# Performance work log

Hardware: AMD Instinct MI355X
Metric: run time of the kernel (lower is better)

## Reference

```python
import jax, jax.numpy as jnp
import numpy as np

N = 50000
E = 400000
IN_DIM = 16
EMB = 32
HID = 128
HEADS = 4
LAYERS = 3
EPS_BN = 1e-5
NEG_SLOPE = 0.2


def setup_inputs() -> dict:
    key = jax.random.key(0)
    ks = jax.random.split(key, 16)
    s = 0.1
    C = HID  # per-head out channels (concat=False)
    inp = {
        "x": jax.random.normal(ks[0], (N, IN_DIM), jnp.float32),
        "edge_index": jax.random.randint(ks[1], (2, E), 0, N, jnp.int64),
        "emb": s * jax.random.normal(ks[2], (N, EMB), jnp.float32),
        "Wf": s * jax.random.normal(ks[3], (EMB, IN_DIM), jnp.float32),
        "bf": jnp.zeros((EMB,), jnp.float32),
        "Wc": s * jax.random.normal(ks[4], (HID, 2 * EMB), jnp.float32),
        "bc": jnp.zeros((HID,), jnp.float32),
        "Wl": s * jax.random.normal(ks[5], (LAYERS, HEADS * C, HID), jnp.float32),
        "a_src": s * jax.random.normal(ks[6], (LAYERS, HEADS, C), jnp.float32),
        "a_dst": s * jax.random.normal(ks[7], (LAYERS, HEADS, C), jnp.float32),
        "bl": jnp.zeros((LAYERS, C), jnp.float32),
        "gamma": jnp.ones((LAYERS, C), jnp.float32),
        "beta": jnp.zeros((LAYERS, C), jnp.float32),
        "Wout": s * jax.random.normal(ks[8], (1, HID), jnp.float32),
        "bout": jnp.zeros((1,), jnp.float32),
    }
    return inp


def _gat_layer(h, src, dst, W, a_s, a_d, b):
    n = h.shape[0]
    C = W.shape[0] // HEADS
    hp = (h @ W.T).reshape(n, HEADS, C)                # (N,H,C)
    al_s = jnp.sum(hp * a_s, axis=-1)                  # (N,H)
    al_d = jnp.sum(hp * a_d, axis=-1)                  # (N,H)
    e = jax.nn.leaky_relu(al_s[src] + al_d[dst], NEG_SLOPE)  # (E,H)
    m = jax.ops.segment_max(e, dst, num_segments=n)    # per-target max
    ex = jnp.exp(e - m[dst])
    denom = jax.ops.segment_sum(ex, dst, num_segments=n) + 1e-16
    alpha = ex / denom[dst]                            # (E,H)
    msg = hp[src] * alpha[..., None]                   # (E,H,C)
    out = jax.ops.segment_sum(msg, dst, num_segments=n)
    return jnp.mean(out, axis=1) + b                   # concat=False: head mean


def _bn(x, g, b):
    mu = jnp.mean(x, axis=0)
    var = jnp.var(x, axis=0)  # biased, as torch BN uses for normalization
    return (x - mu) * jax.lax.rsqrt(var + EPS_BN) * g + b


def reference(x, edge_index, emb, Wf, bf, Wc, bc, Wl, a_src, a_dst, bl, gamma, beta, Wout, bout):
    n = x.shape[0]
    loop = jnp.arange(n, dtype=edge_index.dtype)
    src = jnp.concatenate([edge_index[0], loop])       # add self loops
    dst = jnp.concatenate([edge_index[1], loop])
    feat = x @ Wf.T + bf
    h = jax.nn.relu(jnp.concatenate([emb, feat], axis=1) @ Wc.T + bc)
    prev_h = h
    for i in range(LAYERS):
        h = _gat_layer(h, src, dst, Wl[i], a_src[i], a_dst[i], bl[i])
        h = jax.nn.relu(_bn(h, gamma[i], beta[i]))
        if prev_h.shape == h.shape:
            h = h + prev_h
        prev_h = h
    out = h @ Wout.T + bout
    return jnp.clip(out, -10.0, 10.0)
```

## Files before the change

kernel.cpp:

```cpp
#include <hip/hip_runtime.h>
#include <hip/hip_bf16.h>
#include <math.h>

#define INDIM 16
#define EMBD 32
#define UDIM 64
#define HIDD 128
#define HEADS 4
#define LAYERS 3
#define MPAD 50048

typedef short v8s __attribute__((ext_vector_type(8)));
typedef float v4f __attribute__((ext_vector_type(4)));

__device__ __forceinline__ float lrelu(float x) { return x > 0.f ? x : 0.2f * x; }
__device__ __forceinline__ float bf2f(unsigned int bits16) {
    unsigned int u = bits16 << 16;
    return __builtin_bit_cast(float, u);
}
__device__ __forceinline__ unsigned short f2bf(float f) {
    unsigned int u = __builtin_bit_cast(unsigned int, f);
    unsigned int lsb = (u >> 16) & 1;
    u += 0x7fff + lsb;
    return (unsigned short)(u >> 16);
}

__global__ __launch_bounds__(256) void k_enc(const float* __restrict__ x,
                                             const float* __restrict__ emb,
                                             const float* __restrict__ Wf,
                                             const float* __restrict__ bf,
                                             unsigned short* __restrict__ u, int n) {
    int i = blockIdx.x * 256 + threadIdx.x;
    if (i >= n * EMBD) return;
    int node = i >> 5, j = i & 31;
    const float* xr = x + (size_t)node * INDIM;
    const float* wr = Wf + (size_t)j * INDIM;
    float s = bf[j];
#pragma unroll
    for (int k = 0; k < INDIM; k++) s += xr[k] * wr[k];
    u[(size_t)node * UDIM + EMBD + j] = f2bf(s);
    u[(size_t)node * UDIM + j] = f2bf(emb[(size_t)node * EMBD + j]);
}

__global__ __launch_bounds__(256) void k_prep_v(const float* __restrict__ Wl,
                                                unsigned short* __restrict__ Vb) {
    int i = blockIdx.x * 256 + threadIdx.x;
    if (i >= LAYERS * HIDD * 512) return;
    int l = i >> 16;
    int rem = i & 65535;
    int c = rem >> 9;
    int f = rem & 511;
    int h = f >> 7, k = f & 127;
    Vb[i] = f2bf(Wl[(size_t)l * 512 * HIDD + (size_t)(h * HIDD + c) * HIDD + k]);
}

__global__ __launch_bounds__(256) void k_prep_a(const float* __restrict__ Wl,
                                                const float* __restrict__ a_s,
                                                const float* __restrict__ a_d,
                                                float* __restrict__ ws, float* __restrict__ wd) {
    int i = blockIdx.x * 256 + threadIdx.x;
    if (i >= LAYERS * HEADS * HIDD) return;
    int l = i >> 9, h = (i >> 7) & 3, k = i & 127;
    const float* W = Wl + (size_t)l * 512 * HIDD;
    const float* as = a_s + l * 512 + h * HIDD;
    const float* ad = a_d + l * 512 + h * HIDD;
    float ss = 0.f, sd = 0.f;
    for (int c = 0; c < HIDD; c++) {
        float w = W[(size_t)(h * HIDD + c) * HIDD + k];
        ss += as[c] * w;
        sd += ad[c] * w;
    }
    ws[i] = ss;
    wd[i] = sd;
}

__global__ __launch_bounds__(256) void k_prep_wc(const float* __restrict__ Wc,
                                                 unsigned short* __restrict__ Wcb) {
    int i = blockIdx.x * 256 + threadIdx.x;
    if (i < HIDD * UDIM) Wcb[i] = f2bf(Wc[i]);
}

template <int K, int EPI>
__global__ __launch_bounds__(256) void k_gemm(const unsigned short* __restrict__ A,
                                              const unsigned short* __restrict__ B,
                                              const float* __restrict__ bias,
                                              float* __restrict__ O,
                                              unsigned short* __restrict__ Ob,
                                              float* __restrict__ bns, int M) {
    int tid = threadIdx.x;
    int lane = tid & 63, wid = tid >> 6;
    int wm = wid >> 1, wn = wid & 1;
    int bm = blockIdx.x * 128;
    int lr = lane & 15, lk = lane >> 4;
    __shared__ float s1[128], s2[128];
    if (EPI == 1) {
        if (tid < 128) { s1[tid] = 0.f; s2[tid] = 0.f; }
        __syncthreads();
    }
    v4f acc[4][4] = {};
    const unsigned short* Abase = A + (size_t)(bm + wm * 64 + lr) * K + lk * 8;
    const unsigned short* Bbase = B + (size_t)(wn * 64 + lr) * K + lk * 8;
#pragma unroll
    for (int kk = 0; kk < K / 32; kk++) {
        v8s a[4], b[4];
#pragma unroll
        for (int f = 0; f < 4; f++) {
            a[f] = *(const v8s*)(Abase + (size_t)(f * 16) * K + kk * 32);
            b[f] = *(const v8s*)(Bbase + (size_t)(f * 16) * K + kk * 32);
        }
#pragma unroll
        for (int i = 0; i < 4; i++)
#pragma unroll
            for (int j = 0; j < 4; j++)
                acc[i][j] = __builtin_amdgcn_mfma_f32_16x16x32_bf16(a[i], b[j], acc[i][j], 0, 0, 0);
    }
#pragma unroll
    for (int i = 0; i < 4; i++) {
#pragma unroll
        for (int r = 0; r < 4; r++) {
            int row = bm + wm * 64 + i * 16 + lk * 4 + r;
            if (EPI == 0 && row >= M) continue;
#pragma unroll
            for (int j = 0; j < 4; j++) {
                int col = wn * 64 + j * 16 + lr;
                float v = acc[i][j][r];
                if (EPI == 0) {
                    v = fmaxf(v + bias[col], 0.f);
                    O[(size_t)row * HIDD + col] = v;
                    Ob[(size_t)row * HIDD + col] = f2bf(v);
                } else {
                    O[(size_t)row * HIDD + col] = v;
                }
            }
        }
    }
    if (EPI == 1) {
#pragma unroll
        for (int j = 0; j < 4; j++) {
            int col = wn * 64 + j * 16 + lr;
            float ls = 0.f, lq = 0.f;
#pragma unroll
            for (int i = 0; i < 4; i++)
#pragma unroll
                for (int r = 0; r < 4; r++) {
                    float v = acc[i][j][r];
                    ls += v;
                    lq += v * v;
                }
            atomicAdd(&s1[col], ls);
            atomicAdd(&s2[col], lq);
        }
        __syncthreads();
        if (tid < 128) {
            atomicAdd(&bns[tid], s1[tid]);
            atomicAdd(&bns[128 + tid], s2[tid]);
        }
    }
}

__global__ __launch_bounds__(256) void k_deg(const int* __restrict__ ei, int* __restrict__ deg,
                                             int E, int tot) {
    int e = blockIdx.x * 256 + threadIdx.x;
    if (e >= tot) return;
    int dst = (e < E) ? ei[E + e] : (e - E);
    atomicAdd(&deg[dst], 1);
}

__global__ __launch_bounds__(256) void k_scan1(const int* __restrict__ deg,
                                               int* __restrict__ rowptr,
                                               int* __restrict__ partials, int n) {
    int tid = threadIdx.x;
    int i = blockIdx.x * 256 + tid;
    int v = (i < n) ? deg[i] : 0;
    __shared__ int sm[256];
    sm[tid] = v;
    __syncthreads();
    for (int off = 1; off < 256; off <<= 1) {
        int t = (tid >= off) ? sm[tid - off] : 0;
        __syncthreads();
        sm[tid] += t;
        __syncthreads();
    }
    if (i < n) rowptr[i] = sm[tid] - v;
    if (tid == 255) partials[blockIdx.x] = sm[255];
}

__global__ __launch_bounds__(256) void k_scan2(int* __restrict__ partials, int nb) {
    int tid = threadIdx.x;
    int v = (tid < nb) ? partials[tid] : 0;
    __shared__ int sm[256];
    sm[tid] = v;
    __syncthreads();
    for (int off = 1; off < 256; off <<= 1) {
        int t = (tid >= off) ? sm[tid - off] : 0;
        __syncthreads();
        sm[tid] += t;
        __syncthreads();
    }
    if (tid < nb) partials[tid] = sm[tid] - v;
}

__global__ __launch_bounds__(256) void k_scan3(const int* __restrict__ deg,
                                               const int* __restrict__ partials,
                                               int* __restrict__ rowptr,
                                               int* __restrict__ cursor, int n) {
    int i = blockIdx.x * 256 + threadIdx.x;
    if (i >= n) return;
    int r = rowptr[i] + partials[blockIdx.x];
    rowptr[i] = r;
    cursor[i] = r;
    if (i == n - 1) rowptr[n] = r + deg[i];
}

__global__ __launch_bounds__(256) void k_scatter(const int* __restrict__ ei, int* __restrict__ cursor,
                                                 int* __restrict__ csr_src, int E, int tot) {
    int e = blockIdx.x * 256 + threadIdx.x;
    if (e >= tot) return;
    int src = (e < E) ? ei[e] : (e - E);
    int dst = (e < E) ? ei[E + e] : (e - E);
    int pos = atomicAdd(&cursor[dst], 1);
    csr_src[pos] = src;
}

__global__ __launch_bounds__(256) void k_al0(const float* __restrict__ h,
                                             const float* __restrict__ ws,
                                             const float* __restrict__ wd,
                                             float* __restrict__ al_s, float* __restrict__ al_d,
                                             int n) {
    int wid = threadIdx.x >> 6, lane = threadIdx.x & 63;
    int node = blockIdx.x * 4 + wid;
    if (node >= n) return;
    float2 v = *(const float2*)(h + (size_t)node * HIDD + 2 * lane);
    float s[8];
#pragma unroll
    for (int hh = 0; hh < 4; hh++) {
        float2 w1 = *(const float2*)(ws + hh * HIDD + 2 * lane);
        float2 w2 = *(const float2*)(wd + hh * HIDD + 2 * lane);
        s[hh] = v.x * w1.x + v.y * w1.y;
        s[4 + hh] = v.x * w2.x + v.y * w2.y;
    }
#pragma unroll
    for (int o = 32; o; o >>= 1)
#pragma unroll
        for (int q = 0; q < 8; q++) s[q] += __shfl_xor(s[q], o);
    if (lane == 0) {
        *(float4*)(al_s + (size_t)node * 4) = make_float4(s[0], s[1], s[2], s[3]);
        *(float4*)(al_d + (size_t)node * 4) = make_float4(s[4], s[5], s[6], s[7]);
    }
}

__global__ __launch_bounds__(256) void k_attngat(const int* __restrict__ rowptr,
                                                 const int* __restrict__ csr_src,
                                                 const float* __restrict__ al_s,
                                                 const float* __restrict__ al_d,
                                                 const unsigned short* __restrict__ hb,
                                                 unsigned short* __restrict__ g, int n) {
    int wid = threadIdx.x >> 6, lane = threadIdx.x & 63;
    int node = blockIdx.x * 4 + wid;
    if (node >= n) return;
    int start = rowptr[node], end = rowptr[node + 1];
    int deg = end - start;
    const float4* als4 = (const float4*)al_s;
    float4 ad = ((const float4*)al_d)[node];
    const unsigned int* h2 = (const unsigned int*)hb;
    float acc[4][2] = {};

    if (deg <= 64) {
        bool act = lane < deg;
        int src_l = act ? csr_src[start + lane] : 0;
        float e0 = -3.0e38f, e1 = -3.0e38f, e2 = -3.0e38f, e3 = -3.0e38f;
        if (act) {
            float4 as = als4[src_l];
            e0 = lrelu(as.x + ad.x);
            e1 = lrelu(as.y + ad.y);
            e2 = lrelu(as.z + ad.z);
            e3 = lrelu(as.w + ad.w);
        }
        float m0 = e0, m1 = e1, m2 = e2, m3 = e3;
#pragma unroll
        for (int o = 32; o; o >>= 1) {
            m0 = fmaxf(m0, __shfl_xor(m0, o));
            m1 = fmaxf(m1, __shfl_xor(m1, o));
            m2 = fmaxf(m2, __shfl_xor(m2, o));
            m3 = fmaxf(m3, __shfl_xor(m3, o));
        }
        float p0 = act ? expf(e0 - m0) : 0.f;
        float p1 = act ? expf(e1 - m1) : 0.f;
        float p2 = act ? expf(e2 - m2) : 0.f;
        float p3 = act ? expf(e3 - m3) : 0.f;
        float t0 = p0, t1 = p1, t2 = p2, t3 = p3;
#pragma unroll
        for (int o = 32; o; o >>= 1) {
            t0 += __shfl_xor(t0, o);
            t1 += __shfl_xor(t1, o);
            t2 += __shfl_xor(t2, o);
            t3 += __shfl_xor(t3, o);
        }
        float a0 = p0 / (t0 + 1e-16f), a1 = p1 / (t1 + 1e-16f);
        float a2 = p2 / (t2 + 1e-16f), a3 = p3 / (t3 + 1e-16f);
        for (int jj = 0; jj < deg; jj++) {
            int sj = __shfl(src_l, jj);
            float b0 = __shfl(a0, jj), b1 = __shfl(a1, jj);
            float b2 = __shfl(a2, jj), b3 = __shfl(a3, jj);
            unsigned int uu = h2[(size_t)sj * 64 + lane];
            float x0 = bf2f(uu & 0xffff), x1 = bf2f(uu >> 16);
            acc[0][0] += b0 * x0; acc[0][1] += b0 * x1;
            acc[1][0] += b1 * x0; acc[1][1] += b1 * x1;
            acc[2][0] += b2 * x0; acc[2][1] += b2 * x1;
            acc[3][0] += b3 * x0; acc[3][1] += b3 * x1;
        }
    } else {
        float m0 = -3.0e38f, m1 = -3.0e38f, m2 = -3.0e38f, m3 = -3.0e38f;
        for (int j = start + lane; j < end; j += 64) {
            float4 as = als4[csr_src[j]];
            m0 = fmaxf(m0, lrelu(as.x + ad.x));
            m1 = fmaxf(m1, lrelu(as.y + ad.y));
            m2 = fmaxf(m2, lrelu(as.z + ad.z));
            m3 = fmaxf(m3, lrelu(as.w + ad.w));
        }
#pragma unroll
        for (int o = 32; o; o >>= 1) {
            m0 = fmaxf(m0, __shfl_xor(m0, o));
            m1 = fmaxf(m1, __shfl_xor(m1, o));
            m2 = fmaxf(m2, __shfl_xor(m2, o));
            m3 = fmaxf(m3, __shfl_xor(m3, o));
        }
        float t0 = 0.f, t1 = 0.f, t2 = 0.f, t3 = 0.f;
        for (int j = start + lane; j < end; j += 64) {
            float4 as = als4[csr_src[j]];
            t0 += expf(lrelu(as.x + ad.x) - m0);
            t1 += expf(lrelu(as.y + ad.y) - m1);
            t2 += expf(lrelu(as.z + ad.z) - m2);
            t3 += expf(lrelu(as.w + ad.w) - m3);
        }
#pragma unroll
        for (int o = 32; o; o >>= 1) {
            t0 += __shfl_xor(t0, o);
            t1 += __shfl_xor(t1, o);
            t2 += __shfl_xor(t2, o);
            t3 += __shfl_xor(t3, o);
        }
        float i0 = 1.f / (t0 + 1e-16f), i1 = 1.f / (t1 + 1e-16f);
        float i2 = 1.f / (t2 + 1e-16f), i3 = 1.f / (t3 + 1e-16f);
        for (int base = start; base < end; base += 64) {
            int cnt = min(64, end - base);
            bool act = lane < cnt;
            int src_l = act ? csr_src[base + lane] : 0;
            float a0 = 0.f, a1 = 0.f, a2 = 0.f, a3 = 0.f;
            if (act) {
                float4 as = als4[src_l];
                a0 = expf(lrelu(as.x + ad.x) - m0) * i0;
                a1 = expf(lrelu(as.y + ad.y) - m1) * i1;
                a2 = expf(lrelu(as.z + ad.z) - m2) * i2;
                a3 = expf(lrelu(as.w + ad.w) - m3) * i3;
            }
            for (int jj = 0; jj < cnt; jj++) {
                int sj = __shfl(src_l, jj);
                float b0 = __shfl(a0, jj), b1 = __shfl(a1, jj);
                float b2 = __shfl(a2, jj), b3 = __shfl(a3, jj);
                unsigned int uu = h2[(size_t)sj * 64 + lane];
                float x0 = bf2f(uu & 0xffff), x1 = bf2f(uu >> 16);
                acc[0][0] += b0 * x0; acc[0][1] += b0 * x1;
                acc[1][0] += b1 * x0; acc[1][1] += b1 * x1;
                acc[2][0] += b2 * x0; acc[2][1] += b2 * x1;
                acc[3][0] += b3 * x0; acc[3][1] += b3 * x1;
            }
        }
    }
    unsigned int* g2 = (unsigned int*)g;
#pragma unroll
    for (int hh = 0; hh < 4; hh++) {
        unsigned int p = (unsigned int)f2bf(acc[hh][0]) | ((unsigned int)f2bf(acc[hh][1]) << 16);
        g2[(size_t)node * 256 + hh * 64 + lane] = p;
    }
}

template <int MODE>
__global__ __launch_bounds__(256) void k_apply(const float* __restrict__ agg,
                                               const float* __restrict__ bns,
                                               const float* __restrict__ gamma,
                                               const float* __restrict__ beta,
                                               float* __restrict__ h,
                                               unsigned short* __restrict__ hb,
                                               const float* __restrict__ ws,
                                               const float* __restrict__ wd,
                                               float* __restrict__ al_s,
                                               float* __restrict__ al_d,
                                               const float* __restrict__ Wout,
                                               const float* __restrict__ bout,
                                               float* __restrict__ out,
                                               float invn, int n) {
    int wid = threadIdx.x >> 6, lane = threadIdx.x & 63;
    int node = blockIdx.x * 4 + wid;
    if (node >= n) return;
    int c0 = 2 * lane, c1 = 2 * lane + 1;
    float2 ag = *(const float2*)(agg + (size_t)node * HIDD + c0);
    float2 ho = *(const float2*)(h + (size_t)node * HIDD + c0);
    float mu0 = bns[c0] * invn, mu1 = bns[c1] * invn;
    float va0 = bns[128 + c0] * invn - mu0 * mu0;
    float va1 = bns[128 + c1] * invn - mu1 * mu1;
    float sc0 = gamma[c0] * rsqrtf(0.0625f * va0 + 1e-5f);
    float sc1 = gamma[c1] * rsqrtf(0.0625f * va1 + 1e-5f);
    float v0 = fmaxf((ag.x - mu0) * 0.25f * sc0 + beta[c0], 0.f) + ho.x;
    float v1 = fmaxf((ag.y - mu1) * 0.25f * sc1 + beta[c1], 0.f) + ho.y;
    if (MODE == 0) {
        *(float2*)(h + (size_t)node * HIDD + c0) = make_float2(v0, v1);
        ((unsigned int*)hb)[(size_t)node * 64 + lane] =
            (unsigned int)f2bf(v0) | ((unsigned int)f2bf(v1) << 16);
        float s[8];
#pragma unroll
        for (int hh = 0; hh < 4; hh++) {
            float2 w1 = *(const float2*)(ws + hh * HIDD + c0);
            float2 w2 = *(const float2*)(wd + hh * HIDD + c0);
            s[hh] = v0 * w1.x + v1 * w1.y;
            s[4 + hh] = v0 * w2.x + v1 * w2.y;
        }
#pragma unroll
        for (int o = 32; o; o >>= 1)
#pragma unroll
            for (int q = 0; q < 8; q++) s[q] += __shfl_xor(s[q], o);
        if (lane == 0) {
            *(float4*)(al_s + (size_t)node * 4) = make_float4(s[0], s[1], s[2], s[3]);
            *(float4*)(al_d + (size_t)node * 4) = make_float4(s[4], s[5], s[6], s[7]);
        }
    } else {
        float2 w = *(const float2*)(Wout + c0);
        float p = v0 * w.x + v1 * w.y;
#pragma unroll
        for (int o = 32; o; o >>= 1) p += __shfl_xor(p, o);
        if (lane == 0) {
            float v = p + bout[0];
            out[node] = fminf(fmaxf(v, -10.f), 10.f);
        }
    }
}

extern "C" void kernel_launch(void* const* d_in, const int* in_sizes, int n_in,
                              void* d_out, int out_size, void* d_ws, size_t ws_size,
                              hipStream_t stream) {
    const float* x = (const float*)d_in[0];
    const int* ei = (const int*)d_in[1];
    const float* emb = (const float*)d_in[2];
    const float* Wf = (const float*)d_in[3];
    const float* bf = (const float*)d_in[4];
    const float* Wc = (const float*)d_in[5];
    const float* bc = (const float*)d_in[6];
    const float* Wl = (const float*)d_in[7];
    const float* a_src = (const float*)d_in[8];
    const float* a_dst = (const float*)d_in[9];
    const float* gamma = (const float*)d_in[11];
    const float* beta = (const float*)d_in[12];
    const float* Wout = (const float*)d_in[13];
    const float* bout = (const float*)d_in[14];
    float* out = (float*)d_out;

    int n = in_sizes[0] / INDIM;
    int E = in_sizes[1] / 2;
    int tot = E + n;
    int NB = (n + 255) / 256;

    size_t off = 0;
    auto alloc = [&](size_t bytes) {
        void* p = (char*)d_ws + off;
        off = (off + bytes + 255) & ~(size_t)255;
        return p;
    };
    unsigned short* u = (unsigned short*)alloc((size_t)MPAD * UDIM * 2);
    float* h = (float*)alloc((size_t)MPAD * HIDD * 4);
    unsigned short* hb = (unsigned short*)alloc((size_t)MPAD * HIDD * 2);
    unsigned short* g = (unsigned short*)alloc((size_t)MPAD * 512 * 2);
    float* agg = (float*)alloc((size_t)MPAD * HIDD * 4);
    float* al_s = (float*)alloc((size_t)n * HEADS * 4);
    float* al_d = (float*)alloc((size_t)n * HEADS * 4);
    int* deg = (int*)alloc((size_t)n * 4);
    int* rowptr = (int*)alloc(((size_t)n + 1) * 4);
    int* cursor = (int*)alloc((size_t)n * 4);
    int* csr_src = (int*)alloc((size_t)tot * 4);
    int* partials = (int*)alloc((size_t)NB * 4);
    unsigned short* Vb = (unsigned short*)alloc((size_t)LAYERS * HIDD * 512 * 2);
    unsigned short* Wcb = (unsigned short*)alloc((size_t)HIDD * UDIM * 2);
    float* ws = (float*)alloc((size_t)LAYERS * HEADS * HIDD * 4);
    float* wd = (float*)alloc((size_t)LAYERS * HEADS * HIDD * 4);
    float* bnsums = (float*)alloc(LAYERS * 256 * 4);
    (void)ws_size;

    hipMemsetAsync(deg, 0, (size_t)n * 4, stream);
    hipMemsetAsync(bnsums, 0, LAYERS * 256 * 4, stream);
    if (n < MPAD) {
        hipMemsetAsync(u + (size_t)n * UDIM, 0, (size_t)(MPAD - n) * UDIM * 2, stream);
        hipMemsetAsync(g + (size_t)n * 512, 0, (size_t)(MPAD - n) * 512 * 2, stream);
    }

    k_prep_v<<<(LAYERS * HIDD * 512 + 255) / 256, 256, 0, stream>>>(Wl, Vb);
    k_prep_a<<<(LAYERS * HEADS * HIDD + 255) / 256, 256, 0, stream>>>(Wl, a_src, a_dst, ws, wd);
    k_prep_wc<<<(HIDD * UDIM + 255) / 256, 256, 0, stream>>>(Wc, Wcb);

    k_deg<<<(tot + 255) / 256, 256, 0, stream>>>(ei, deg, E, tot);
    k_scan1<<<NB, 256, 0, stream>>>(deg, rowptr, partials, n);
    k_scan2<<<1, 256, 0, stream>>>(partials, NB);
    k_scan3<<<NB, 256, 0, stream>>>(deg, partials, rowptr, cursor, n);
    k_scatter<<<(tot + 255) / 256, 256, 0, stream>>>(ei, cursor, csr_src, E, tot);

    k_enc<<<(n * EMBD + 255) / 256, 256, 0, stream>>>(x, emb, Wf, bf, u, n);
    k_gemm<UDIM, 0><<<MPAD / 128, 256, 0, stream>>>(u, Wcb, bc, h, hb, nullptr, n);
    k_al0<<<(n + 3) / 4, 256, 0, stream>>>(h, ws, wd, al_s, al_d, n);

    float invn = 1.0f / (float)n;
    for (int l = 0; l < LAYERS; l++) {
        k_attngat<<<(n + 3) / 4, 256, 0, stream>>>(rowptr, csr_src, al_s, al_d, hb, g, n);
        k_gemm<512, 1><<<MPAD / 128, 256, 0, stream>>>(g, Vb + (size_t)l * HIDD * 512, nullptr,
                                                       agg, nullptr, bnsums + l * 256, MPAD);
        if (l < LAYERS - 1)
            k_apply<0><<<(n + 3) / 4, 256, 0, stream>>>(
                agg, bnsums + l * 256, gamma + l * HIDD, beta + l * HIDD, h, hb,
                ws + (size_t)(l + 1) * 512, wd + (size_t)(l + 1) * 512, al_s, al_d,
                nullptr, nullptr, nullptr, invn, n);
        else
            k_apply<1><<<(n + 3) / 4, 256, 0, stream>>>(
                agg, bnsums + l * 256, gamma + l * HIDD, beta + l * HIDD, h, hb,
                nullptr, nullptr, nullptr, nullptr, Wout, bout, out, invn, n);
    }
}
```

Measured before the change: 486.3 us.

## Fuse GAT attention aggregation with projection GEMM through shared memory

Merges the attention-aggregation kernel and the per-layer 512-wide projection GEMM into a single kernel. Each block aggregates 16 nodes into a bf16 tile in LDS, then multiplies it by the weight matrix with MFMA and accumulates the batch-norm statistics. This removes the round trip of the N×512 bf16 intermediate through global memory and one launch per layer. The neighbor gather loop is also unrolled by two to raise memory-level parallelism. In exchange, the weight matrix is re-read from global/L2 by every 16-row block, the MFMA tile is small, and the per-block BN atomics grow because there are many more blocks.

```diff
diff --git a/kernel.cpp b/kernel.cpp
--- a/kernel.cpp
+++ b/kernel.cpp
@@ -80,23 +80,17 @@
     if (i < HIDD * UDIM) Wcb[i] = f2bf(Wc[i]);
 }
 
-template <int K, int EPI>
-__global__ __launch_bounds__(256) void k_gemm(const unsigned short* __restrict__ A,
-                                              const unsigned short* __restrict__ B,
-                                              const float* __restrict__ bias,
-                                              float* __restrict__ O,
-                                              unsigned short* __restrict__ Ob,
-                                              float* __restrict__ bns, int M) {
+__global__ __launch_bounds__(256) void k_gemm_enc(const unsigned short* __restrict__ A,
+                                                  const unsigned short* __restrict__ B,
+                                                  const float* __restrict__ bias,
+                                                  float* __restrict__ O,
+                                                  unsigned short* __restrict__ Ob, int M) {
+    const int K = UDIM;
     int tid = threadIdx.x;
     int lane = tid & 63, wid = tid >> 6;
     int wm = wid >> 1, wn = wid & 1;
     int bm = blockIdx.x * 128;
     int lr = lane & 15, lk = lane >> 4;
-    __shared__ float s1[128], s2[128];
-    if (EPI == 1) {
-        if (tid < 128) { s1[tid] = 0.f; s2[tid] = 0.f; }
-        __syncthreads();
-    }
     v4f acc[4][4] = {};
     const unsigned short* Abase = A + (size_t)(bm + wm * 64 + lr) * K + lk * 8;
     const unsigned short* Bbase = B + (size_t)(wn * 64 + lr) * K + lk * 8;
@@ -119,41 +113,14 @@
 #pragma unroll
         for (int r = 0; r < 4; r++) {
             int row = bm + wm * 64 + i * 16 + lk * 4 + r;
-            if (EPI == 0 && row >= M) continue;
+            if (row >= M) continue;
 #pragma unroll
             for (int j = 0; j < 4; j++) {
                 int col = wn * 64 + j * 16 + lr;
-                float v = acc[i][j][r];
-                if (EPI == 0) {
-                    v = fmaxf(v + bias[col], 0.f);
-                    O[(size_t)row * HIDD + col] = v;
-                    Ob[(size_t)row * HIDD + col] = f2bf(v);
-                } else {
-                    O[(size_t)row * HIDD + col] = v;
-                }
+                float v = fmaxf(acc[i][j][r] + bias[col], 0.f);
+                O[(size_t)row * HIDD + col] = v;
+                Ob[(size_t)row * HIDD + col] = f2bf(v);
             }
-        }
-    }
-    if (EPI == 1) {
-#pragma unroll
-        for (int j = 0; j < 4; j++) {
-            int col = wn * 64 + j * 16 + lr;
-            float ls = 0.f, lq = 0.f;
-#pragma unroll
-            for (int i = 0; i < 4; i++)
-#pragma unroll
-                for (int r = 0; r < 4; r++) {
-                    float v = acc[i][j][r];
-                    ls += v;
-                    lq += v * v;
-                }
-            atomicAdd(&s1[col], ls);
-            atomicAdd(&s2[col], lq);
-        }
-        __syncthreads();
-        if (tid < 128) {
-            atomicAdd(&bns[tid], s1[tid]);
-            atomicAdd(&bns[128 + tid], s2[tid]);
         }
     }
 }
@@ -249,129 +216,189 @@
     }
 }
 
-__global__ __launch_bounds__(256) void k_attngat(const int* __restrict__ rowptr,
-                                                 const int* __restrict__ csr_src,
-                                                 const float* __restrict__ al_s,
-                                                 const float* __restrict__ al_d,
-                                                 const unsigned short* __restrict__ hb,
-                                                 unsigned short* __restrict__ g, int n) {
-    int wid = threadIdx.x >> 6, lane = threadIdx.x & 63;
-    int node = blockIdx.x * 4 + wid;
-    if (node >= n) return;
-    int start = rowptr[node], end = rowptr[node + 1];
-    int deg = end - start;
+__global__ __launch_bounds__(256) void k_layer(const int* __restrict__ rowptr,
+                                               const int* __restrict__ csr_src,
+                                               const float* __restrict__ al_s,
+                                               const float* __restrict__ al_d,
+                                               const unsigned short* __restrict__ hb,
+                                               const unsigned short* __restrict__ Vb,
+                                               float* __restrict__ agg,
+                                               float* __restrict__ bns, int n) {
+    __shared__ unsigned short G[16][520];
+    __shared__ float s1[128], s2[128];
+    int tid = threadIdx.x, lane = tid & 63, wid = tid >> 6;
+    if (tid < 128) { s1[tid] = 0.f; s2[tid] = 0.f; }
+    int node0 = blockIdx.x * 16;
     const float4* als4 = (const float4*)al_s;
-    float4 ad = ((const float4*)al_d)[node];
     const unsigned int* h2 = (const unsigned int*)hb;
-    float acc[4][2] = {};
-
-    if (deg <= 64) {
-        bool act = lane < deg;
-        int src_l = act ? csr_src[start + lane] : 0;
-        float e0 = -3.0e38f, e1 = -3.0e38f, e2 = -3.0e38f, e3 = -3.0e38f;
-        if (act) {
-            float4 as = als4[src_l];
-            e0 = lrelu(as.x + ad.x);
-            e1 = lrelu(as.y + ad.y);
-            e2 = lrelu(as.z + ad.z);
-            e3 = lrelu(as.w + ad.w);
-        }
-        float m0 = e0, m1 = e1, m2 = e2, m3 = e3;
-#pragma unroll
-        for (int o = 32; o; o >>= 1) {
-            m0 = fmaxf(m0, __shfl_xor(m0, o));
-            m1 = fmaxf(m1, __shfl_xor(m1, o));
-            m2 = fmaxf(m2, __shfl_xor(m2, o));
-            m3 = fmaxf(m3, __shfl_xor(m3, o));
-        }
-        float p0 = act ? expf(e0 - m0) : 0.f;
-        float p1 = act ? expf(e1 - m1) : 0.f;
-        float p2 = act ? expf(e2 - m2) : 0.f;
-        float p3 = act ? expf(e3 - m3) : 0.f;
-        float t0 = p0, t1 = p1, t2 = p2, t3 = p3;
-#pragma unroll
-        for (int o = 32; o; o >>= 1) {
-            t0 += __shfl_xor(t0, o);
-            t1 += __shfl_xor(t1, o);
-            t2 += __shfl_xor(t2, o);
-            t3 += __shfl_xor(t3, o);
-        }
-        float a0 = p0 / (t0 + 1e-16f), a1 = p1 / (t1 + 1e-16f);
-        float a2 = p2 / (t2 + 1e-16f), a3 = p3 / (t3 + 1e-16f);
-        for (int jj = 0; jj < deg; jj++) {
-            int sj = __shfl(src_l, jj);
-            float b0 = __shfl(a0, jj), b1 = __shfl(a1, jj);
-            float b2 = __shfl(a2, jj), b3 = __shfl(a3, jj);
-            unsigned int uu = h2[(size_t)sj * 64 + lane];
-            float x0 = bf2f(uu & 0xffff), x1 = bf2f(uu >> 16);
-            acc[0][0] += b0 * x0; acc[0][1] += b0 * x1;
-            acc[1][0] += b1 * x0; acc[1][1] += b1 * x1;
-            acc[2][0] += b2 * x0; acc[2][1] += b2 * x1;
-            acc[3][0] += b3 * x0; acc[3][1] += b3 * x1;
-        }
-    } else {
-        float m0 = -3.0e38f, m1 = -3.0e38f, m2 = -3.0e38f, m3 = -3.0e38f;
-        for (int j = start + lane; j < end; j += 64) {
-            float4 as = als4[csr_src[j]];
-            m0 = fmaxf(m0, lrelu(as.x + ad.x));
-            m1 = fmaxf(m1, lrelu(as.y + ad.y));
-            m2 = fmaxf(m2, lrelu(as.z + ad.z));
-            m3 = fmaxf(m3, lrelu(as.w + ad.w));
-        }
-#pragma unroll
-        for (int o = 32; o; o >>= 1) {
-            m0 = fmaxf(m0, __shfl_xor(m0, o));
-            m1 = fmaxf(m1, __shfl_xor(m1, o));
-            m2 = fmaxf(m2, __shfl_xor(m2, o));
-            m3 = fmaxf(m3, __shfl_xor(m3, o));
-        }
-        float t0 = 0.f, t1 = 0.f, t2 = 0.f, t3 = 0.f;
-        for (int j = start + lane; j < end; j += 64) {
-            float4 as = als4[csr_src[j]];
-            t0 += expf(lrelu(as.x + ad.x) - m0);
-            t1 += expf(lrelu(as.y + ad.y) - m1);
-            t2 += expf(lrelu(as.z + ad.z) - m2);
-            t3 += expf(lrelu(as.w + ad.w) - m3);
-        }
-#pragma unroll
-        for (int o = 32; o; o >>= 1) {
-            t0 += __shfl_xor(t0, o);
-            t1 += __shfl_xor(t1, o);
-            t2 += __shfl_xor(t2, o);
-            t3 += __shfl_xor(t3, o);
-        }
-        float i0 = 1.f / (t0 + 1e-16f), i1 = 1.f / (t1 + 1e-16f);
-        float i2 = 1.f / (t2 + 1e-16f), i3 = 1.f / (t3 + 1e-16f);
-        for (int base = start; base < end; base += 64) {
-            int cnt = min(64, end - base);
-            bool act = lane < cnt;
-            int src_l = act ? csr_src[base + lane] : 0;
-            float a0 = 0.f, a1 = 0.f, a2 = 0.f, a3 = 0.f;
-            if (act) {
-                float4 as = als4[src_l];
-                a0 = expf(lrelu(as.x + ad.x) - m0) * i0;
-                a1 = expf(lrelu(as.y + ad.y) - m1) * i1;
-                a2 = expf(lrelu(as.z + ad.z) - m2) * i2;
-                a3 = expf(lrelu(as.w + ad.w) - m3) * i3;
+    unsigned int* Gw = (unsigned int*)G;
+
+    for (int i = 0; i < 4; i++) {
+        int lrow = wid * 4 + i;
+        int node = node0 + lrow;
+        float acc[4][2] = {};
+        if (node < n) {
+            int start = rowptr[node], end = rowptr[node + 1];
+            int deg = end - start;
+            float4 ad = ((const float4*)al_d)[node];
+            if (deg <= 64) {
+                bool act = lane < deg;
+                int src_l = act ? csr_src[start + lane] : 0;
+                float e0 = -3.0e38f, e1 = -3.0e38f, e2 = -3.0e38f, e3 = -3.0e38f;
+                if (act) {
+                    float4 as = als4[src_l];
+                    e0 = lrelu(as.x + ad.x);
+                    e1 = lrelu(as.y + ad.y);
+                    e2 = lrelu(as.z + ad.z);
+                    e3 = lrelu(as.w + ad.w);
+                }
+                float m0 = e0, m1 = e1, m2 = e2, m3 = e3;
+#pragma unroll
+                for (int o = 32; o; o >>= 1) {
+                    m0 = fmaxf(m0, __shfl_xor(m0, o));
+                    m1 = fmaxf(m1, __shfl_xor(m1, o));
+                    m2 = fmaxf(m2, __shfl_xor(m2, o));
+                    m3 = fmaxf(m3, __shfl_xor(m3, o));
+                }
+                float p0 = act ? expf(e0 - m0) : 0.f;
+                float p1 = act ? expf(e1 - m1) : 0.f;
+                float p2 = act ? expf(e2 - m2) : 0.f;
+                float p3 = act ? expf(e3 - m3) : 0.f;
+                float t0 = p0, t1 = p1, t2 = p2, t3 = p3;
+#pragma unroll
+                for (int o = 32; o; o >>= 1) {
+                    t0 += __shfl_xor(t0, o);
+                    t1 += __shfl_xor(t1, o);
+                    t2 += __shfl_xor(t2, o);
+                    t3 += __shfl_xor(t3, o);
+                }
+                float a0 = p0 / (t0 + 1e-16f), a1 = p1 / (t1 + 1e-16f);
+                float a2 = p2 / (t2 + 1e-16f), a3 = p3 / (t3 + 1e-16f);
+                int jj = 0;
+                for (; jj + 2 <= deg; jj += 2) {
+                    int sj0 = __shfl(src_l, jj), sj1 = __shfl(src_l, jj + 1);
+                    unsigned int u0 = h2[(size_t)sj0 * 64 + lane];
+                    unsigned int u1 = h2[(size_t)sj1 * 64 + lane];
+                    float b00 = __shfl(a0, jj), b01 = __shfl(a1, jj);
+                    float b02 = __shfl(a2, jj), b03 = __shfl(a3, jj);
+                    float b10 = __shfl(a0, jj + 1), b11 = __shfl(a1, jj + 1);
+                    float b12 = __shfl(a2, jj + 1), b13 = __shfl(a3, jj + 1);
+                    float x00 = bf2f(u0 & 0xffff), x01 = bf2f(u0 >> 16);
+                    float x10 = bf2f(u1 & 0xffff), x11 = bf2f(u1 >> 16);
+                    acc[0][0] += b00 * x00 + b10 * x10; acc[0][1] += b00 * x01 + b10 * x11;
+                    acc[1][0] += b01 * x00 + b11 * x10; acc[1][1] += b01 * x01 + b11 * x11;
+                    acc[2][0] += b02 * x00 + b12 * x10; acc[2][1] += b02 * x01 + b12 * x11;
+                    acc[3][0] += b03 * x00 + b13 * x10; acc[3][1] += b03 * x01 + b13 * x11;
+                }
+                if (jj < deg) {
+                    int sj = __shfl(src_l, jj);
+                    unsigned int uu = h2[(size_t)sj * 64 + lane];
+                    float b0 = __shfl(a0, jj), b1 = __shfl(a1, jj);
+                    float b2 = __shfl(a2, jj), b3 = __shfl(a3, jj);
+                    float x0 = bf2f(uu & 0xffff), x1 = bf2f(uu >> 16);
+                    acc[0][0] += b0 * x0; acc[0][1] += b0 * x1;
+                    acc[1][0] += b1 * x0; acc[1][1] += b1 * x1;
+                    acc[2][0] += b2 * x0; acc[2][1] += b2 * x1;
+                    acc[3][0] += b3 * x0; acc[3][1] += b3 * x1;
+                }
+            } else {
+                float m0 = -3.0e38f, m1 = -3.0e38f, m2 = -3.0e38f, m3 = -3.0e38f;
+                for (int j = start + lane; j < end; j += 64) {
+                    float4 as = als4[csr_src[j]];
+                    m0 = fmaxf(m0, lrelu(as.x + ad.x));
+                    m1 = fmaxf(m1, lrelu(as.y + ad.y));
+                    m2 = fmaxf(m2, lrelu(as.z + ad.z));
+                    m3 = fmaxf(m3, lrelu(as.w + ad.w));
+                }
+#pragma unroll
+                for (int o = 32; o; o >>= 1) {
+                    m0 = fmaxf(m0, __shfl_xor(m0, o));
+                    m1 = fmaxf(m1, __shfl_xor(m1, o));
+                    m2 = fmaxf(m2, __shfl_xor(m2, o));
+                    m3 = fmaxf(m3, __shfl_xor(m3, o));
+                }
+                float t0 = 0.f, t1 = 0.f, t2 = 0.f, t3 = 0.f;
+                for (int j = start + lane; j < end; j += 64) {
+                    float4 as = als4[csr_src[j]];
+                    t0 += expf(lrelu(as.x + ad.x) - m0);
+                    t1 += expf(lrelu(as.y + ad.y) - m1);
+                    t2 += expf(lrelu(as.z + ad.z) - m2);
+                    t3 += expf(lrelu(as.w + ad.w) - m3);
+                }
+#pragma unroll
+                for (int o = 32; o; o >>= 1) {
+                    t0 += __shfl_xor(t0, o);
+                    t1 += __shfl_xor(t1, o);
+                    t2 += __shfl_xor(t2, o);
+                    t3 += __shfl_xor(t3, o);
+                }
+                float i0 = 1.f / (t0 + 1e-16f), i1 = 1.f / (t1 + 1e-16f);
+                float i2 = 1.f / (t2 + 1e-16f), i3 = 1.f / (t3 + 1e-16f);
+                for (int base = start; base < end; base += 64) {
+                    int cnt = min(64, end - base);
+                    bool act = lane < cnt;
+                    int src_l = act ? csr_src[base + lane] : 0;
+                    float a0 = 0.f, a1 = 0.f, a2 = 0.f, a3 = 0.f;
+                    if (act) {
+                        float4 as = als4[src_l];
+                        a0 = expf(lrelu(as.x + ad.x) - m0) * i0;
+                        a1 = expf(lrelu(as.y + ad.y) - m1) * i1;
+                        a2 = expf(lrelu(as.z + ad.z) - m2) * i2;
+                        a3 = expf(lrelu(as.w + ad.w) - m3) * i3;
+                    }
+                    for (int jj = 0; jj < cnt; jj++) {
+                        int sj = __shfl(src_l, jj);
+                        float b0 = __shfl(a0, jj), b1 = __shfl(a1, jj);
+                        float b2 = __shfl(a2, jj), b3 = __shfl(a3, jj);
+                        unsigned int uu = h2[(size_t)sj * 64 + lane];
+                        float x0 = bf2f(uu & 0xffff), x1 = bf2f(uu >> 16);
+                        acc[0][0] += b0 * x0; acc[0][1] += b0 * x1;
+                        acc[1][0] += b1 * x0; acc[1][1] += b1 * x1;
+                        acc[2][0] += b2 * x0; acc[2][1] += b2 * x1;
+                        acc[3][0] += b3 * x0; acc[3][1] += b3 * x1;
+                    }
+                }
             }
-            for (int jj = 0; jj < cnt; jj++) {
-                int sj = __shfl(src_l, jj);
-                float b0 = __shfl(a0, jj), b1 = __shfl(a1, jj);
-                float b2 = __shfl(a2, jj), b3 = __shfl(a3, jj);
-                unsigned int uu = h2[(size_t)sj * 64 + lane];
-                float x0 = bf2f(uu & 0xffff), x1 = bf2f(uu >> 16);
-                acc[0][0] += b0 * x0; acc[0][1] += b0 * x1;
-                acc[1][0] += b1 * x0; acc[1][1] += b1 * x1;
-                acc[2][0] += b2 * x0; acc[2][1] += b2 * x1;
-                acc[3][0] += b3 * x0; acc[3][1] += b3 * x1;
+        }
+#pragma unroll
+        for (int hh = 0; hh < 4; hh++) {
+            unsigned int p = (unsigned int)f2bf(acc[hh][0]) | ((unsigned int)f2bf(acc[hh][1]) << 16);
+            Gw[lrow * 260 + hh * 64 + lane] = p;
+        }
+    }
+    __syncthreads();
+
+    int lr = lane & 15, lk = lane >> 4;
+    v4f acc2[2] = {};
+#pragma unroll
+    for (int kk = 0; kk < 16; kk++) {
+        v8s a = *(const v8s*)((const char*)G + lr * 1040 + kk * 64 + lk * 16);
+        v8s b0 = *(const v8s*)(Vb + (size_t)(wid * 32 + lr) * 512 + kk * 32 + lk * 8);
+        v8s b1 = *(const v8s*)(Vb + (size_t)(wid * 32 + 16 + lr) * 512 + kk * 32 + lk * 8);
+        acc2[0] = __builtin_amdgcn_mfma_f32_16x16x32_bf16(a, b0, acc2[0], 0, 0, 0);
+        acc2[1] = __builtin_amdgcn_mfma_f32_16x16x32_bf16(a, b1, acc2[1], 0, 0, 0);
+    }
+#pragma unroll
+    for (int j = 0; j < 2; j++) {
+        int col = wid * 32 + j * 16 + lr;
+        float ls = 0.f, lq = 0.f;
+#pragma unroll
+        for (int r = 0; r < 4; r++) {
+            int node = node0 + lk * 4 + r;
+            float v = acc2[j][r];
+            if (node < n) {
+                agg[(size_t)node * HIDD + col] = v;
+                ls += v;
+                lq += v * v;
             }
         }
-    }
-    unsigned int* g2 = (unsigned int*)g;
-#pragma unroll
-    for (int hh = 0; hh < 4; hh++) {
-        unsigned int p = (unsigned int)f2bf(acc[hh][0]) | ((unsigned int)f2bf(acc[hh][1]) << 16);
-        g2[(size_t)node * 256 + hh * 64 + lane] = p;
+        atomicAdd(&s1[col], ls);
+        atomicAdd(&s2[col], lq);
+    }
+    __syncthreads();
+    if (tid < 128) {
+        atomicAdd(&bns[tid], s1[tid]);
+        atomicAdd(&bns[128 + tid], s2[tid]);
     }
 }
 
@@ -468,7 +495,6 @@
     unsigned short* u = (unsigned short*)alloc((size_t)MPAD * UDIM * 2);
     float* h = (float*)alloc((size_t)MPAD * HIDD * 4);
     unsigned short* hb = (unsigned short*)alloc((size_t)MPAD * HIDD * 2);
-    unsigned short* g = (unsigned short*)alloc((size_t)MPAD * 512 * 2);
     float* agg = (float*)alloc((size_t)MPAD * HIDD * 4);
     float* al_s = (float*)alloc((size_t)n * HEADS * 4);
     float* al_d = (float*)alloc((size_t)n * HEADS * 4);
@@ -488,7 +514,6 @@
     hipMemsetAsync(bnsums, 0, LAYERS * 256 * 4, stream);
     if (n < MPAD) {
         hipMemsetAsync(u + (size_t)n * UDIM, 0, (size_t)(MPAD - n) * UDIM * 2, stream);
-        hipMemsetAsync(g + (size_t)n * 512, 0, (size_t)(MPAD - n) * 512 * 2, stream);
     }
 
     k_prep_v<<<(LAYERS * HIDD * 512 + 255) / 256, 256, 0, stream>>>(Wl, Vb);
@@ -502,14 +527,15 @@
     k_scatter<<<(tot + 255) / 256, 256, 0, stream>>>(ei, cursor, csr_src, E, tot);
 
     k_enc<<<(n * EMBD + 255) / 256, 256, 0, stream>>>(x, emb, Wf, bf, u, n);
-    k_gemm<UDIM, 0><<<MPAD / 128, 256, 0, stream>>>(u, Wcb, bc, h, hb, nullptr, n);
+    k_gemm_enc<<<MPAD / 128, 256, 0, stream>>>(u, Wcb, bc, h, hb, n);
     k_al0<<<(n + 3) / 4, 256, 0, stream>>>(h, ws, wd, al_s, al_d, n);
 
     float invn = 1.0f / (float)n;
+    int NLB = (n + 15) / 16;
     for (int l = 0; l < LAYERS; l++) {
-        k_attngat<<<(n + 3) / 4, 256, 0, stream>>>(rowptr, csr_src, al_s, al_d, hb, g, n);
-        k_gemm<512, 1><<<MPAD / 128, 256, 0, stream>>>(g, Vb + (size_t)l * HIDD * 512, nullptr,
-                                                       agg, nullptr, bnsums + l * 256, MPAD);
+        k_layer<<<NLB, 256, 0, stream>>>(rowptr, csr_src, al_s, al_d, hb,
+                                         Vb + (size_t)l * HIDD * 512, agg,
+                                         bnsums + l * 256, n);
         if (l < LAYERS - 1)
             k_apply<0><<<(n + 3) / 4, 256, 0, stream>>>(
                 agg, bnsums + l * 256, gamma + l * HIDD, beta + l * HIDD, h, hb,
```

Result: slower. 525.3 us (+8.0%).
